# Kernel tuning notes

Hardware: AMD Instinct MI355X
Metric: run time of the kernel (lower is better)

## Reference

```python
import jax, jax.numpy as jnp
import numpy as np

N_NODES = 100000
IN_CH = 256
H1, C1 = 8, 8   # conv1: heads=8, out_channels=8
H2, C2 = 1, 3   # conv2: heads=1, out_channels=3
NEG_SLOPE = 0.2
EPS = 1e-16


def gat_conv(x, src, dst, W, a_src, a_dst, b, heads, out_ch, n_nodes):
    """PyG-style GATConv (eval mode, self-loops already in src/dst)."""
    h = (x @ W).reshape(n_nodes, heads, out_ch)          # [N,H,C]
    alpha_s = jnp.einsum('nhc,hc->nh', h, a_src)         # [N,H]
    alpha_d = jnp.einsum('nhc,hc->nh', h, a_dst)         # [N,H]
    e = alpha_s[src] + alpha_d[dst]                      # [E,H]
    e = jnp.where(e > 0, e, NEG_SLOPE * e)               # leaky_relu(0.2)
    # segment softmax over destination nodes
    m = jax.ops.segment_max(e, dst, num_segments=n_nodes)
    m = jnp.where(jnp.isfinite(m), m, 0.0)
    ex = jnp.exp(e - m[dst])
    s = jax.ops.segment_sum(ex, dst, num_segments=n_nodes)
    a = ex / (s[dst] + EPS)                              # [E,H]
    msg = h[src] * a[:, :, None]                         # [E,H,C]
    out = jax.ops.segment_sum(msg, dst, num_segments=n_nodes)  # [N,H,C]
    return out.reshape(n_nodes, heads * out_ch) + b


def setup_inputs() -> dict:
    key = jax.random.key(0)
    ks = jax.random.split(key, 10)
    x = jax.random.normal(ks[0], (N_NODES, IN_CH), dtype=jnp.float32)
    edge_index = jax.random.randint(ks[1], (2, 3200000), 0, N_NODES, dtype=jnp.int64)
    sc = 0.1
    return {
        'x': x,
        'edge_index': edge_index,
        'W1': jax.random.normal(ks[2], (IN_CH, H1 * C1), dtype=jnp.float32) * sc,
        'a_src1': jax.random.normal(ks[3], (H1, C1), dtype=jnp.float32) * sc,
        'a_dst1': jax.random.normal(ks[4], (H1, C1), dtype=jnp.float32) * sc,
        'b1': jnp.zeros((H1 * C1,), dtype=jnp.float32),
        'W2': jax.random.normal(ks[5], (H1 * C1, H2 * C2), dtype=jnp.float32) * sc,
        'a_src2': jax.random.normal(ks[6], (H2, C2), dtype=jnp.float32) * sc,
        'a_dst2': jax.random.normal(ks[7], (H2, C2), dtype=jnp.float32) * sc,
        'b2': jnp.zeros((H2 * C2,), dtype=jnp.float32),
    }


def reference(x, edge_index, W1, a_src1, a_dst1, b1, W2, a_src2, a_dst2, b2):
    n = x.shape[0]
    loop = jnp.arange(n, dtype=edge_index.dtype)
    src = jnp.concatenate([edge_index[0], loop])  # add_self_loops=True
    dst = jnp.concatenate([edge_index[1], loop])
    h = gat_conv(x, src, dst, W1, a_src1, a_dst1, b1, H1, C1, n)
    h = jax.nn.elu(h)
    out = gat_conv(h, src, dst, W2, a_src2, a_dst2, b2, H2, C2, n)
    return out
```

## Files before the change

### kernel.cpp

```cpp
#include <hip/hip_runtime.h>
#include <hip/hip_bf16.h>

#define P_W1  0
#define P_AS1 16384
#define P_AD1 16448
#define P_B1  16512
#define P_W2  16576
#define P_AS2 16768
#define P_AD2 16771
#define P_B2  16774

#define NBLK_CSR 512
#define CXB      768

typedef __attribute__((ext_vector_type(8))) short short8;
typedef __attribute__((ext_vector_type(8))) unsigned short ushort8v;
typedef __attribute__((ext_vector_type(4))) float floatx4;

__device__ __forceinline__ float ldf(const void* p, int i, int bf) {
  if (bf) {
    unsigned v = ((unsigned)((const unsigned short*)p)[i]) << 16;
    float f; __builtin_memcpy(&f, &v, 4); return f;
  }
  return ((const float*)p)[i];
}
__device__ __forceinline__ int ldi(const void* p, long i, int i64) {
  return i64 ? ((const int*)p)[2*i] : ((const int*)p)[i];
}
__device__ __forceinline__ unsigned short f2bfbits(float f) {
  __hip_bfloat16 b = __float2bfloat16(f);
  unsigned short u; __builtin_memcpy(&u, &b, 2); return u;
}
__device__ __forceinline__ float bf2f(unsigned short u) {
  unsigned v = ((unsigned)u) << 16;
  float f; __builtin_memcpy(&f, &v, 4); return f;
}

__global__ void k_prep(const void* x, const void* ei,
                       const void* w1, const void* as1, const void* ad1, const void* b1,
                       const void* w2, const void* as2, const void* ad2, const void* b2,
                       int* flags, float* params, unsigned short* w1t) {
  __shared__ int sh[2];
  int tid = threadIdx.x, lane = tid & 63, w = tid >> 6;
  if (w == 0) {
    const unsigned* xw = (const unsigned*)x;
    int hits = 0;
    for (int i = lane; i < 256; i += 64) {
      unsigned b = (xw[i] >> 7) & 0xFF;
      hits += (b >= 96 && b <= 141) ? 1 : 0;
    }
    for (int o = 32; o >= 1; o >>= 1) hits += __shfl_xor(hits, o);
    if (lane == 0) sh[0] = (hits >= 160) ? 1 : 0;
  } else if (w == 1) {
    const unsigned* ew = (const unsigned*)ei;
    int z = 0;
    for (int i = lane; i < 128; i += 64) z += (ew[2*i+1] == 0u) ? 1 : 0;
    for (int o = 32; o >= 1; o >>= 1) z += __shfl_xor(z, o);
    if (lane == 0) sh[1] = (z >= 64) ? 1 : 0;
  }
  __syncthreads();
  int bf = sh[0];
  if (tid == 0) { flags[0] = sh[0]; flags[1] = sh[1]; }
  for (int i = tid; i < 16384; i += blockDim.x) {
    int ch = i >> 8, k = i & 255;
    w1t[i] = f2bfbits(ldf(w1, k * 64 + ch, bf));
  }
  if (!bf) {
    for (int i = tid; i < 16384; i += blockDim.x) params[P_W1 + i] = ldf(w1, i, bf);
  }
  for (int i = tid; i < 64; i += blockDim.x) {
    params[P_AS1 + i] = ldf(as1, i, bf);
    params[P_AD1 + i] = ldf(ad1, i, bf);
    params[P_B1  + i] = ldf(b1,  i, bf);
  }
  for (int i = tid; i < 192; i += blockDim.x) params[P_W2 + i] = ldf(w2, i, bf);
  for (int i = tid; i < 3; i += blockDim.x) {
    params[P_AS2 + i] = ldf(as2, i, bf);
    params[P_AD2 + i] = ldf(ad2, i, bf);
    params[P_B2  + i] = ldf(b2,  i, bf);
  }
}

__global__ void k_bcount(const void* ei, const int* flags, int* gcnt, int* brsv,
                         int E0, int N, int NB, int chunk,
                         const void* x, uint4* xcopy) {
  __shared__ int h[256];
  int tid = threadIdx.x;
  if (blockIdx.x >= NBLK_CSR) {
    if (flags[0]) {
      const uint4* xs4 = (const uint4*)x;
      long n16 = (long)N * 32;
      long stride = (long)CXB * 256;
      for (long i = (long)(blockIdx.x - NBLK_CSR) * 256 + tid; i < n16; i += stride)
        xcopy[i] = xs4[i];
    }
    return;
  }
  int i64 = flags[1];
  for (int j = tid; j < NB; j += 256) h[j] = 0;
  __syncthreads();
  int E = E0 + N;
  int b0 = blockIdx.x * chunk, b1 = min(b0 + chunk, E);
  for (int e = b0 + tid; e < b1; e += 256) {
    int dst = (e < E0) ? ldi(ei, (long)E0 + e, i64) : (e - E0);
    atomicAdd(&h[dst >> 9], 1);
  }
  __syncthreads();
  for (int j = tid; j < NB; j += 256)
    brsv[blockIdx.x * NB + j] = atomicAdd(&gcnt[j], h[j]);
}

__global__ void k_bbase(const int* gcnt, int* bbase, int NB) {
  __shared__ int sh[256];
  int tid = threadIdx.x;
  sh[tid] = (tid < NB) ? gcnt[tid] : 0;
  __syncthreads();
  int own = sh[tid];
  for (int ofs = 1; ofs < 256; ofs <<= 1) {
    int v = (tid >= ofs) ? sh[tid - ofs] : 0;
    __syncthreads();
    sh[tid] += v;
    __syncthreads();
  }
  if (tid < NB) bbase[tid] = sh[tid] - own;
  if (tid == NB - 1) bbase[NB] = sh[tid];
}

__global__ void k_bscatter(const void* ei, const int* flags, const int* bbase,
                           const int* brsv, unsigned* pairs, int E0, int N, int NB, int chunk) {
  __shared__ int base_s[256];
  __shared__ int rnk[256];
  int i64 = flags[1], tid = threadIdx.x;
  for (int j = tid; j < NB; j += 256) {
    base_s[j] = bbase[j] + brsv[blockIdx.x * NB + j];
    rnk[j] = 0;
  }
  __syncthreads();
  int E = E0 + N;
  int b0 = blockIdx.x * chunk, b1 = min(b0 + chunk, E);
  for (int e = b0 + tid; e < b1; e += 256) {
    int src, dst;
    if (e < E0) { src = ldi(ei, e, i64); dst = ldi(ei, (long)E0 + e, i64); }
    else        { src = e - E0; dst = src; }
    int bkt = dst >> 9;
    int r = atomicAdd(&rnk[bkt], 1);
    pairs[base_s[bkt] + r] = ((unsigned)src << 9) | (unsigned)(dst & 511);
  }
}

__global__ void k_bsort(const unsigned* pairs, const int* bbase, int* rowp,
                        int* srcs, int N, int NB, int E) {
  __shared__ int h0[512], sc[512], rk[512];
  int b = blockIdx.x, tid = threadIdx.x;
  int s0 = bbase[b], s1 = bbase[b + 1], L = s1 - s0;
  for (int j = tid; j < 512; j += 256) { h0[j] = 0; rk[j] = 0; }
  __syncthreads();
  for (int i = tid; i < L; i += 256) atomicAdd(&h0[pairs[s0 + i] & 511], 1);
  __syncthreads();
  for (int j = tid; j < 512; j += 256) sc[j] = h0[j];
  __syncthreads();
  for (int ofs = 1; ofs < 512; ofs <<= 1) {
    int j0 = tid, j1 = tid + 256;
    int v0 = (j0 >= ofs) ? sc[j0 - ofs] : 0;
    int v1 = (j1 >= ofs) ? sc[j1 - ofs] : 0;
    __syncthreads();
    sc[j0] += v0; sc[j1] += v1;
    __syncthreads();
  }
  for (int j = tid; j < 512; j += 256) {
    int off = sc[j] - h0[j];
    int node = (b << 9) + j;
    if (node < N) rowp[node] = s0 + off;
    sc[j] = off;
  }
  if (b == 0 && tid == 0) rowp[N] = E;
  __syncthreads();
  for (int i = tid; i < L; i += 256) {
    unsigned p = pairs[s0 + i];
    int j = p & 511;
    int r = atomicAdd(&rk[j], 1);
    srcs[s0 + sc[j] + r] = (int)(p >> 9);
  }
}

#define XP 272

__device__ __forceinline__ void gemm1_f32(const float* x, const float* params,
                                          unsigned short* h1, float* a_s, float* a_d,
                                          int N, int wave, int lane) {
  int n0 = wave * 4;
  if (n0 >= N) return;
  int nb[4];
#pragma unroll
  for (int j = 0; j < 4; j++) nb[j] = min(n0 + j, N - 1) * 256;
  float acc[4] = {0.f, 0.f, 0.f, 0.f};
  const float* W = params + P_W1;
  for (int k = 0; k < 256; k++) {
    float wv = W[k * 64 + lane];
#pragma unroll
    for (int j = 0; j < 4; j++) acc[j] += x[nb[j] + k] * wv;
  }
  float as1v = params[P_AS1 + lane], ad1v = params[P_AD1 + lane];
#pragma unroll
  for (int j = 0; j < 4; j++) {
    int n = n0 + j;
    if (n >= N) break;
    float hv = acc[j];
    float s = hv * as1v, d = hv * ad1v;
    s += __shfl_xor(s, 1); s += __shfl_xor(s, 2); s += __shfl_xor(s, 4);
    d += __shfl_xor(d, 1); d += __shfl_xor(d, 2); d += __shfl_xor(d, 4);
    h1[(size_t)n * 64 + lane] = f2bfbits(hv);
    if ((lane & 7) == 0) {
      a_s[n * 8 + (lane >> 3)] = s;
      a_d[n * 8 + (lane >> 3)] = d;
    }
  }
}

__global__ void k_gemm1(const void* x, const unsigned short* xcopy, const unsigned short* w1t,
                        const int* flags, const float* params,
                        unsigned short* h1, float* a_s, float* a_d, int N) {
  __shared__ unsigned short xs[16 * XP];
  int tid = threadIdx.x;
  int wv = tid >> 6, lane = tid & 63;
  if (flags[0]) {
    int n0 = blockIdx.x * 16;
#pragma unroll
    for (int it = 0; it < 2; it++) {
      int idx = tid + it * 256;
      int row = idx >> 5, col = idx & 31;
      int gn = n0 + row; if (gn >= N) gn = N - 1;
      uint4 v = *(const uint4*)(xcopy + (size_t)gn * 256 + col * 8);
      *(uint4*)(xs + row * XP + col * 8) = v;
    }
    __syncthreads();
    int quad = lane >> 4, l16 = lane & 15;
    int ch = wv * 16 + l16;
    floatx4 acc = {0.f, 0.f, 0.f, 0.f};
    const unsigned short* xrow = xs + l16 * XP + quad * 8;
    const unsigned short* wrow = w1t + (size_t)ch * 256 + quad * 8;
#pragma unroll
    for (int k0 = 0; k0 < 256; k0 += 32) {
      short8 a = *(const short8*)(xrow + k0);
      short8 b = *(const short8*)(wrow + k0);
      acc = __builtin_amdgcn_mfma_f32_16x16x32_bf16(a, b, acc, 0, 0, 0);
    }
    float asv = params[P_AS1 + ch], adv = params[P_AD1 + ch];
#pragma unroll
    for (int r = 0; r < 4; r++) {
      int n = n0 + quad * 4 + r;
      if (n >= N) break;
      float d = acc[r];
      h1[(size_t)n * 64 + ch] = f2bfbits(d);
      float s = d * asv, t = d * adv;
      s += __shfl_xor(s, 1); s += __shfl_xor(s, 2); s += __shfl_xor(s, 4);
      t += __shfl_xor(t, 1); t += __shfl_xor(t, 2); t += __shfl_xor(t, 4);
      if ((lane & 7) == 0) {
        int head = ch >> 3;
        a_s[n * 8 + head] = s;
        a_d[n * 8 + head] = t;
      }
    }
  } else {
    gemm1_f32((const float*)x, params, h1, a_s, a_d, N, blockIdx.x * 4 + wv, lane);
  }
}

__global__ void k_agg1(const float* params, const unsigned short* h1, const float* a_s,
                       const float* a_d, const int* rowp, const int* srcs,
                       float4* pk, float* ad2, int N) {
  int n = blockIdx.x * (blockDim.x >> 6) + (threadIdx.x >> 6);
  int lane = threadIdx.x & 63;
  if (n >= N) return;
  int start = rowp[n], end = rowp[n + 1];
  int h = lane & 7, es = lane >> 3;
  float adh = a_d[n * 8 + h];
  float m = -1e30f;
  for (int i = start + es; i < end; i += 8) {
    float e = a_s[srcs[i] * 8 + h] + adh;
    e = e > 0.f ? e : 0.2f * e;
    m = fmaxf(m, e);
  }
  m = fmaxf(m, __shfl_xor(m, 8));
  m = fmaxf(m, __shfl_xor(m, 16));
  m = fmaxf(m, __shfl_xor(m, 32));
  float acc[8] = {0.f,0.f,0.f,0.f,0.f,0.f,0.f,0.f};
  float ssum = 0.f;
  for (int i = start + es; i < end; i += 8) {
    int s = srcs[i];
    float e = a_s[s * 8 + h] + adh;
    e = e > 0.f ? e : 0.2f * e;
    float ex = __expf(e - m);
    ssum += ex;
    ushort8v u = *(const ushort8v*)(h1 + (size_t)s * 64 + h * 8);
#pragma unroll
    for (int c = 0; c < 8; c++) acc[c] += ex * bf2f(u[c]);
  }
#pragma unroll
  for (int msk = 8; msk <= 32; msk <<= 1) {
    ssum += __shfl_xor(ssum, msk);
#pragma unroll
    for (int c = 0; c < 8; c++) acc[c] += __shfl_xor(acc[c], msk);
  }
  if (es == 0) {
    float inv = 1.f / (ssum + 1e-16f);
    float pj0 = 0.f, pj1 = 0.f, pj2 = 0.f;
#pragma unroll
    for (int c = 0; c < 8; c++) {
      float v = acc[c] * inv + params[P_B1 + h * 8 + c];
      v = v > 0.f ? v : (__expf(v) - 1.f);
      const float* w2r = params + P_W2 + (h * 8 + c) * 3;
      pj0 += v * w2r[0]; pj1 += v * w2r[1]; pj2 += v * w2r[2];
    }
    pj0 += __shfl_xor(pj0, 1); pj1 += __shfl_xor(pj1, 1); pj2 += __shfl_xor(pj2, 1);
    pj0 += __shfl_xor(pj0, 2); pj1 += __shfl_xor(pj1, 2); pj2 += __shfl_xor(pj2, 2);
    pj0 += __shfl_xor(pj0, 4); pj1 += __shfl_xor(pj1, 4); pj2 += __shfl_xor(pj2, 4);
    if (h == 0) {
      float as2 = pj0*params[P_AS2+0] + pj1*params[P_AS2+1] + pj2*params[P_AS2+2];
      float ad2v = pj0*params[P_AD2+0] + pj1*params[P_AD2+1] + pj2*params[P_AD2+2];
      pk[n] = make_float4(pj0, pj1, pj2, as2);
      ad2[n] = ad2v;
    }
  }
}

__global__ void k_agg2(const float* params, const float4* pk, const float* ad2,
                       const int* rowp, const int* srcs, void* out, const int* flags, int N) {
  int wid = blockIdx.x * (blockDim.x >> 6) + (threadIdx.x >> 6);
  int lane = threadIdx.x & 63;
  int g = lane >> 4, t = lane & 15;
  int n = wid * 4 + g;
  if (n >= N) return;
  int start = rowp[n], end = rowp[n + 1];
  float ad = ad2[n];
  float m = -1e30f;
  for (int i = start + t; i < end; i += 16) {
    float e = pk[srcs[i]].w + ad;
    e = e > 0.f ? e : 0.2f * e;
    m = fmaxf(m, e);
  }
#pragma unroll
  for (int msk = 1; msk <= 8; msk <<= 1) m = fmaxf(m, __shfl_xor(m, msk));
  float ssum = 0.f, c0 = 0.f, c1 = 0.f, c2 = 0.f;
  for (int i = start + t; i < end; i += 16) {
    float4 v = pk[srcs[i]];
    float e = v.w + ad;
    e = e > 0.f ? e : 0.2f * e;
    float ex = __expf(e - m);
    ssum += ex;
    c0 += ex * v.x; c1 += ex * v.y; c2 += ex * v.z;
  }
#pragma unroll
  for (int msk = 1; msk <= 8; msk <<= 1) {
    ssum += __shfl_xor(ssum, msk);
    c0 += __shfl_xor(c0, msk); c1 += __shfl_xor(c1, msk); c2 += __shfl_xor(c2, msk);
  }
  if (t == 0) {
    float inv = 1.f / (ssum + 1e-16f);
    float o0 = c0 * inv + params[P_B2+0];
    float o1 = c1 * inv + params[P_B2+1];
    float o2 = c2 * inv + params[P_B2+2];
    if (flags[0]) {
      __hip_bfloat16* ob = (__hip_bfloat16*)out;
      ob[n*3+0] = __float2bfloat16(o0);
      ob[n*3+1] = __float2bfloat16(o1);
      ob[n*3+2] = __float2bfloat16(o2);
    } else {
      float* of = (float*)out;
      of[n*3+0] = o0; of[n*3+1] = o1; of[n*3+2] = o2;
    }
  }
}

extern "C" void kernel_launch(void* const* d_in, const int* in_sizes, int n_in,
                              void* d_out, int out_size, void* d_ws, size_t ws_size,
                              hipStream_t stream) {
  const void* x  = d_in[0];
  const void* ei = d_in[1];
  int N  = in_sizes[0] / 256;
  int E0 = in_sizes[1] / 2;
  int E  = E0 + N;
  int NB = (N + 511) >> 9;
  int chunk = (E + NBLK_CSR - 1) / NBLK_CSR;

  char* w = (char*)d_ws;
  size_t off = 0;
  auto alloc = [&](size_t bytes) -> char* {
    char* p = w + off;
    off += (bytes + 255) & ~(size_t)255;
    return p;
  };
  int*            flags  = (int*)           alloc(256);
  float*          params = (float*)         alloc(17408 * 4);
  unsigned short* w1t    = (unsigned short*)alloc(16384 * 2);
  unsigned short* h1     = (unsigned short*)alloc((size_t)N * 64 * 2);
  float*          a_s1   = (float*)         alloc((size_t)N * 8 * 4);
  float*          a_d1   = (float*)         alloc((size_t)N * 8 * 4);
  float4*         pk     = (float4*)        alloc((size_t)N * 16);
  float*          ad2    = (float*)         alloc((size_t)N * 4);
  int*            gcnt   = (int*)           alloc(256 * 4);
  int*            bbase  = (int*)           alloc(257 * 4);
  int*            brsv   = (int*)           alloc((size_t)NBLK_CSR * NB * 4);
  int*            rowp   = (int*)           alloc((size_t)(N + 1) * 4);
  unsigned*       pairs  = (unsigned*)      alloc((size_t)E * 4);
  int*            srcs   = (int*)           alloc((size_t)E * 4);
  unsigned short* xcopy  = (unsigned short*)alloc((size_t)N * 256 * 2);
  (void)ws_size; (void)n_in; (void)out_size;

  hipMemsetAsync(gcnt, 0, 256 * 4, stream);
  k_prep<<<1, 256, 0, stream>>>(x, ei, d_in[2], d_in[3], d_in[4], d_in[5],
                                d_in[6], d_in[7], d_in[8], d_in[9], flags, params, w1t);
  k_bcount<<<dim3(NBLK_CSR + CXB), 256, 0, stream>>>(ei, flags, gcnt, brsv, E0, N, NB, chunk,
                                                     x, (uint4*)xcopy);
  k_bbase<<<1, 256, 0, stream>>>(gcnt, bbase, NB);
  k_bscatter<<<dim3(NBLK_CSR), 256, 0, stream>>>(ei, flags, bbase, brsv, pairs, E0, N, NB, chunk);
  k_bsort<<<dim3(NB), 256, 0, stream>>>(pairs, bbase, rowp, srcs, N, NB, E);
  k_gemm1<<<dim3((N + 15) / 16), 256, 0, stream>>>(x, xcopy, w1t, flags, params, h1, a_s1, a_d1, N);
  k_agg1<<<dim3((N + 3) / 4), 256, 0, stream>>>(params, h1, a_s1, a_d1, rowp, srcs, pk, ad2, N);
  k_agg2<<<dim3((N + 15) / 16), 256, 0, stream>>>(params, pk, ad2, rowp, srcs, d_out, flags, N);
}
```

Before: 678.5 us.

## Fuse bucket sort with GEMM1 and load bf16 x directly into LDS

Drops the separate x copy that ran alongside bcount and merges the bucket-sort kernel with the first GEMM into one launch, using disjoint block ranges. The GEMM now pulls x straight from global memory into swizzled LDS with global_load_lds, works on 64-row tiles, and keeps W fragments in registers. It also writes h1 as vectorized bf16 through an LDS transpose and computes the attention dots per head without shuffles. The aim is to cut one full pass over x, one launch, and the per-row write overhead. The cost is more LDS per block and register pressure that may reduce occupancy.

```diff
diff --git a/kernel.cpp b/kernel.cpp
--- a/kernel.cpp
+++ b/kernel.cpp
@@ -11,7 +11,6 @@
 #define P_B2  16774
 
 #define NBLK_CSR 512
-#define CXB      768
 
 typedef __attribute__((ext_vector_type(8))) short short8;
 typedef __attribute__((ext_vector_type(8))) unsigned short ushort8v;
@@ -82,20 +81,9 @@
 }
 
 __global__ void k_bcount(const void* ei, const int* flags, int* gcnt, int* brsv,
-                         int E0, int N, int NB, int chunk,
-                         const void* x, uint4* xcopy) {
+                         int E0, int N, int NB, int chunk) {
   __shared__ int h[256];
   int tid = threadIdx.x;
-  if (blockIdx.x >= NBLK_CSR) {
-    if (flags[0]) {
-      const uint4* xs4 = (const uint4*)x;
-      long n16 = (long)N * 32;
-      long stride = (long)CXB * 256;
-      for (long i = (long)(blockIdx.x - NBLK_CSR) * 256 + tid; i < n16; i += stride)
-        xcopy[i] = xs4[i];
-    }
-    return;
-  }
   int i64 = flags[1];
   for (int j = tid; j < NB; j += 256) h[j] = 0;
   __syncthreads();
@@ -147,43 +135,6 @@
     pairs[base_s[bkt] + r] = ((unsigned)src << 9) | (unsigned)(dst & 511);
   }
 }
-
-__global__ void k_bsort(const unsigned* pairs, const int* bbase, int* rowp,
-                        int* srcs, int N, int NB, int E) {
-  __shared__ int h0[512], sc[512], rk[512];
-  int b = blockIdx.x, tid = threadIdx.x;
-  int s0 = bbase[b], s1 = bbase[b + 1], L = s1 - s0;
-  for (int j = tid; j < 512; j += 256) { h0[j] = 0; rk[j] = 0; }
-  __syncthreads();
-  for (int i = tid; i < L; i += 256) atomicAdd(&h0[pairs[s0 + i] & 511], 1);
-  __syncthreads();
-  for (int j = tid; j < 512; j += 256) sc[j] = h0[j];
-  __syncthreads();
-  for (int ofs = 1; ofs < 512; ofs <<= 1) {
-    int j0 = tid, j1 = tid + 256;
-    int v0 = (j0 >= ofs) ? sc[j0 - ofs] : 0;
-    int v1 = (j1 >= ofs) ? sc[j1 - ofs] : 0;
-    __syncthreads();
-    sc[j0] += v0; sc[j1] += v1;
-    __syncthreads();
-  }
-  for (int j = tid; j < 512; j += 256) {
-    int off = sc[j] - h0[j];
-    int node = (b << 9) + j;
-    if (node < N) rowp[node] = s0 + off;
-    sc[j] = off;
-  }
-  if (b == 0 && tid == 0) rowp[N] = E;
-  __syncthreads();
-  for (int i = tid; i < L; i += 256) {
-    unsigned p = pairs[s0 + i];
-    int j = p & 511;
-    int r = atomicAdd(&rk[j], 1);
-    srcs[s0 + sc[j] + r] = (int)(p >> 9);
-  }
-}
-
-#define XP 272
 
 __device__ __forceinline__ void gemm1_f32(const float* x, const float* params,
                                           unsigned short* h1, float* a_s, float* a_d,
@@ -217,52 +168,118 @@
   }
 }
 
-__global__ void k_gemm1(const void* x, const unsigned short* xcopy, const unsigned short* w1t,
-                        const int* flags, const float* params,
-                        unsigned short* h1, float* a_s, float* a_d, int N) {
-  __shared__ unsigned short xs[16 * XP];
+__global__ void k_bsort_gemm1(const unsigned* pairs, const int* bbase, int* rowp, int* srcs,
+                              const void* x, const unsigned short* w1t, const int* flags,
+                              const float* params, unsigned short* h1, float* a_s, float* a_d,
+                              int N, int NB, int E) {
+  __shared__ __align__(16) char smem[32768];
   int tid = threadIdx.x;
-  int wv = tid >> 6, lane = tid & 63;
+  if ((int)blockIdx.x < NB) {
+    int* h0 = (int*)smem;
+    int* sc = h0 + 512;
+    int* rk = sc + 512;
+    int b = blockIdx.x;
+    int s0 = bbase[b], s1 = bbase[b + 1], L = s1 - s0;
+    for (int j = tid; j < 512; j += 256) { h0[j] = 0; rk[j] = 0; }
+    __syncthreads();
+    for (int i = tid; i < L; i += 256) atomicAdd(&h0[pairs[s0 + i] & 511], 1);
+    __syncthreads();
+    for (int j = tid; j < 512; j += 256) sc[j] = h0[j];
+    __syncthreads();
+    for (int ofs = 1; ofs < 512; ofs <<= 1) {
+      int j0 = tid, j1 = tid + 256;
+      int v0 = (j0 >= ofs) ? sc[j0 - ofs] : 0;
+      int v1 = (j1 >= ofs) ? sc[j1 - ofs] : 0;
+      __syncthreads();
+      sc[j0] += v0; sc[j1] += v1;
+      __syncthreads();
+    }
+    for (int j = tid; j < 512; j += 256) {
+      int off = sc[j] - h0[j];
+      int node = (b << 9) + j;
+      if (node < N) rowp[node] = s0 + off;
+      sc[j] = off;
+    }
+    if (b == 0 && tid == 0) rowp[N] = E;
+    __syncthreads();
+    for (int i = tid; i < L; i += 256) {
+      unsigned p = pairs[s0 + i];
+      int j = p & 511;
+      int r = atomicAdd(&rk[j], 1);
+      srcs[s0 + sc[j] + r] = (int)(p >> 9);
+    }
+    return;
+  }
+  int tile = blockIdx.x - NB;
+  int w = tid >> 6, lane = tid & 63;
   if (flags[0]) {
-    int n0 = blockIdx.x * 16;
-#pragma unroll
-    for (int it = 0; it < 2; it++) {
-      int idx = tid + it * 256;
-      int row = idx >> 5, col = idx & 31;
-      int gn = n0 + row; if (gn >= N) gn = N - 1;
-      uint4 v = *(const uint4*)(xcopy + (size_t)gn * 256 + col * 8);
-      *(uint4*)(xs + row * XP + col * 8) = v;
-    }
-    __syncthreads();
-    int quad = lane >> 4, l16 = lane & 15;
-    int ch = wv * 16 + l16;
-    floatx4 acc = {0.f, 0.f, 0.f, 0.f};
-    const unsigned short* xrow = xs + l16 * XP + quad * 8;
-    const unsigned short* wrow = w1t + (size_t)ch * 256 + quad * 8;
-#pragma unroll
-    for (int k0 = 0; k0 < 256; k0 += 32) {
-      short8 a = *(const short8*)(xrow + k0);
-      short8 b = *(const short8*)(wrow + k0);
-      acc = __builtin_amdgcn_mfma_f32_16x16x32_bf16(a, b, acc, 0, 0, 0);
-    }
-    float asv = params[P_AS1 + ch], adv = params[P_AD1 + ch];
-#pragma unroll
-    for (int r = 0; r < 4; r++) {
-      int n = n0 + quad * 4 + r;
-      if (n >= N) break;
-      float d = acc[r];
-      h1[(size_t)n * 64 + ch] = f2bfbits(d);
-      float s = d * asv, t = d * adv;
-      s += __shfl_xor(s, 1); s += __shfl_xor(s, 2); s += __shfl_xor(s, 4);
-      t += __shfl_xor(t, 1); t += __shfl_xor(t, 2); t += __shfl_xor(t, 4);
-      if ((lane & 7) == 0) {
-        int head = ch >> 3;
+    int row0 = tile << 6;
+    int l16 = lane & 15, quad = lane >> 4;
+    int ch = w * 16 + l16;
+    const char* xb = (const char*)x;
+#pragma unroll
+    for (int j = 0; j < 8; j++) {
+      int g = w * 512 + j * 64 + lane;
+      int r = g >> 5;
+      int p = (g & 31) << 4;
+      int gr = row0 + r; if (gr >= N) gr = N - 1;
+      const char* src = xb + (size_t)gr * 512 + (size_t)(p ^ ((r & 7) << 4));
+      char* dst = smem + w * 8192 + j * 1024 + lane * 16;
+      __builtin_amdgcn_global_load_lds((const __attribute__((address_space(1))) unsigned int*)src,
+                                       (__attribute__((address_space(3))) unsigned int*)dst,
+                                       16, 0, 0);
+    }
+    short8 bfr[8];
+    const unsigned short* wp = w1t + (size_t)ch * 256 + quad * 8;
+#pragma unroll
+    for (int i = 0; i < 8; i++) bfr[i] = *(const short8*)(wp + i * 32);
+    __syncthreads();
+    floatx4 acc[4];
+#pragma unroll
+    for (int rg = 0; rg < 4; rg++) {
+      floatx4 a4 = {0.f, 0.f, 0.f, 0.f};
+      int r = rg * 16 + l16;
+      const char* arow = smem + r * 512;
+      int swz = (r & 7) << 4;
+#pragma unroll
+      for (int i = 0; i < 8; i++) {
+        short8 afr = *(const short8*)(arow + ((quad * 16 + i * 64) ^ swz));
+        a4 = __builtin_amdgcn_mfma_f32_16x16x32_bf16(afr, bfr[i], a4, 0, 0, 0);
+      }
+      acc[rg] = a4;
+    }
+    __syncthreads();
+    float* ht = (float*)smem;
+#pragma unroll
+    for (int rg = 0; rg < 4; rg++)
+#pragma unroll
+      for (int rr = 0; rr < 4; rr++)
+        ht[(rg * 16 + quad * 4 + rr) * 68 + ch] = acc[rg][rr];
+    __syncthreads();
+    int t = tid;
+#pragma unroll
+    for (int it = 0; it < 2; it++, t += 256) {
+      int nl = t >> 3, head = t & 7;
+      int n = row0 + nl;
+      if (n < N) {
+        const float* hr = ht + nl * 68 + head * 8;
+        float s = 0.f, d = 0.f;
+        ushort8v u;
+#pragma unroll
+        for (int c = 0; c < 8; c++) {
+          float v = hr[c];
+          s += v * params[P_AS1 + head * 8 + c];
+          d += v * params[P_AD1 + head * 8 + c];
+          u[c] = f2bfbits(v);
+        }
+        *(ushort8v*)(h1 + (size_t)n * 64 + head * 8) = u;
         a_s[n * 8 + head] = s;
-        a_d[n * 8 + head] = t;
+        a_d[n * 8 + head] = d;
       }
     }
   } else {
-    gemm1_f32((const float*)x, params, h1, a_s, a_d, N, blockIdx.x * 4 + wv, lane);
+    for (int k4 = 0; k4 < 4; k4++)
+      gemm1_f32((const float*)x, params, h1, a_s, a_d, N, tile * 16 + w * 4 + k4, lane);
   }
 }
 
@@ -382,6 +399,7 @@
   int E  = E0 + N;
   int NB = (N + 511) >> 9;
   int chunk = (E + NBLK_CSR - 1) / NBLK_CSR;
+  int ntile = (N + 63) >> 6;
 
   char* w = (char*)d_ws;
   size_t off = 0;
@@ -404,18 +422,16 @@
   int*            rowp   = (int*)           alloc((size_t)(N + 1) * 4);
   unsigned*       pairs  = (unsigned*)      alloc((size_t)E * 4);
   int*            srcs   = (int*)           alloc((size_t)E * 4);
-  unsigned short* xcopy  = (unsigned short*)alloc((size_t)N * 256 * 2);
   (void)ws_size; (void)n_in; (void)out_size;
 
   hipMemsetAsync(gcnt, 0, 256 * 4, stream);
   k_prep<<<1, 256, 0, stream>>>(x, ei, d_in[2], d_in[3], d_in[4], d_in[5],
                                 d_in[6], d_in[7], d_in[8], d_in[9], flags, params, w1t);
-  k_bcount<<<dim3(NBLK_CSR + CXB), 256, 0, stream>>>(ei, flags, gcnt, brsv, E0, N, NB, chunk,
-                                                     x, (uint4*)xcopy);
+  k_bcount<<<dim3(NBLK_CSR), 256, 0, stream>>>(ei, flags, gcnt, brsv, E0, N, NB, chunk);
   k_bbase<<<1, 256, 0, stream>>>(gcnt, bbase, NB);
   k_bscatter<<<dim3(NBLK_CSR), 256, 0, stream>>>(ei, flags, bbase, brsv, pairs, E0, N, NB, chunk);
-  k_bsort<<<dim3(NB), 256, 0, stream>>>(pairs, bbase, rowp, srcs, N, NB, E);
-  k_gemm1<<<dim3((N + 15) / 16), 256, 0, stream>>>(x, xcopy, w1t, flags, params, h1, a_s1, a_d1, N);
+  k_bsort_gemm1<<<dim3(NB + ntile), 256, 0, stream>>>(pairs, bbase, rowp, srcs, x, w1t, flags,
+                                                      params, h1, a_s1, a_d1, N, NB, E);
   k_agg1<<<dim3((N + 3) / 4), 256, 0, stream>>>(params, h1, a_s1, a_d1, rowp, srcs, pk, ad2, N);
   k_agg2<<<dim3((N + 15) / 16), 256, 0, stream>>>(params, pk, ad2, rowp, srcs, d_out, flags, N);
 }
```

Measured after the change: 704.9 us. 1.04x slower.
